# Performance work log

Hardware: AMD Instinct MI355X
Metric: run time of the kernel (lower is better)

## Reference

```python
import jax, jax.numpy as jnp
import numpy as np

NT, C, B, N, H, E = 32768, 128, 64, 512, 4, 524288  # total nodes, channels, graphs, nodes/graph, heads, edges
DH = C // H
EPS = 1e-5


def batchnorm(x, g, b):
    # BatchNorm1d over the node dimension (training-mode batch statistics)
    m = x.mean(axis=0)
    v = x.var(axis=0)
    return (x - m) * jax.lax.rsqrt(v + EPS) * g + b


def setup_inputs() -> dict:
    key = jax.random.key(0)
    ks = jax.random.split(key, 8)
    s = 1.0 / np.sqrt(C)
    return dict(
        x=jax.random.normal(ks[0], (NT, C), jnp.float32),
        edge_index=jax.random.randint(ks[1], (2, E), 0, NT, dtype=jnp.int32),
        Wc=jax.random.normal(ks[2], (C, C), jnp.float32) * s,
        bc=jnp.zeros((C,), jnp.float32),
        in_proj_w=jax.random.normal(ks[3], (3 * C, C), jnp.float32) * s,
        in_proj_b=jnp.zeros((3 * C,), jnp.float32),
        out_proj_w=jax.random.normal(ks[4], (C, C), jnp.float32) * s,
        out_proj_b=jnp.zeros((C,), jnp.float32),
        gn1=jnp.ones((C,), jnp.float32), bn1=jnp.zeros((C,), jnp.float32),
        gn2=jnp.ones((C,), jnp.float32), bn2=jnp.zeros((C,), jnp.float32),
        gn3=jnp.ones((C,), jnp.float32), bn3=jnp.zeros((C,), jnp.float32),
        Wm1=jax.random.normal(ks[5], (2 * C, C), jnp.float32) * s,
        bm1=jnp.zeros((2 * C,), jnp.float32),
        Wm2=jax.random.normal(ks[6], (C, 2 * C), jnp.float32) / np.sqrt(2 * C),
        bm2=jnp.zeros((C,), jnp.float32),
    )


def reference(x, edge_index, Wc, bc, in_proj_w, in_proj_b, out_proj_w, out_proj_b,
              gn1, bn1, gn2, bn2, gn3, bn3, Wm1, bm1, Wm2, bm2):
    # --- local branch: mean-aggregation message passing + linear + residual + BN ---
    src, dst = edge_index[0], edge_index[1]
    agg = jax.ops.segment_sum(x[src], dst, num_segments=NT)            # [NT, C]
    cnt = jax.ops.segment_sum(jnp.ones((E, 1), x.dtype), dst, num_segments=NT)
    agg = agg / jnp.maximum(cnt, 1.0)
    h_local = agg @ Wc.T + bc + x                                       # dropout p=0 -> no-op
    h_local = batchnorm(h_local, gn1, bn1)

    # --- global branch: to_dense_batch (equal-size graphs -> reshape) + MHA ---
    hd = x.reshape(B, N, C)
    qkv = hd @ in_proj_w.T + in_proj_b                                  # [B, N, 3C]
    q, k, v = jnp.split(qkv, 3, axis=-1)
    q = q.reshape(B, N, H, DH).transpose(0, 2, 1, 3)                    # [B, H, N, DH]
    k = k.reshape(B, N, H, DH).transpose(0, 2, 1, 3)
    v = v.reshape(B, N, H, DH).transpose(0, 2, 1, 3)
    scores = jnp.einsum('bhqd,bhkd->bhqk', q, k) / np.sqrt(DH)          # [B, H, N, N]
    attn = jax.nn.softmax(scores, axis=-1)
    o = jnp.einsum('bhqk,bhkd->bhqd', attn, v)                          # [B, H, N, DH]
    o = o.transpose(0, 2, 1, 3).reshape(B, N, C)
    h_attn = (o @ out_proj_w.T + out_proj_b).reshape(NT, C) + x
    h_attn = batchnorm(h_attn, gn2, bn2)

    # --- combine + MLP + final norm ---
    out = h_local + h_attn
    out = out + (jax.nn.relu(out @ Wm1.T + bm1) @ Wm2.T + bm2)
    return batchnorm(out, gn3, bn3)
```

## Files before the change

### kernel.cpp

```cpp
#include <hip/hip_runtime.h>
#include <cstddef>

#define NT    32768
#define CCH   128
#define BB    64
#define NNODE 512
#define NHEAD 4
#define DHEAD 32
#define EE    524288
#define EPS   1e-5f
#define MAXDEG 96
#define CURPAD 16
#define SSLOT  8
#define EGRP  2048
#define FILL0 2128

typedef unsigned short u16;
typedef unsigned int   u32;
typedef __attribute__((ext_vector_type(8))) short short8;
typedef __attribute__((ext_vector_type(4))) short short4v;
typedef __attribute__((ext_vector_type(4))) float f32x4;

__device__ __forceinline__ float b2f(u32 w) { return __uint_as_float(w << 16); }
__device__ __forceinline__ u16 f2b(float f) {
    u32 u = __float_as_uint(f);
    u += 0x7FFF + ((u >> 16) & 1);
    return (u16)(u >> 16);
}
__device__ __forceinline__ u32 cvtpk(float lo, float hi) {
    u32 r;
    asm("v_cvt_pk_bf16_f32 %0, %1, %2" : "=v"(r) : "v"(lo), "v"(hi));
    return r;
}
#if __has_builtin(__builtin_amdgcn_exp2f)
#define EXP2(x) __builtin_amdgcn_exp2f(x)
#else
#define EXP2(x) exp2f(x)
#endif
#define SCLOG2E (0.1767766952966369f * 1.4426950408889634f)

__global__ __launch_bounds__(256) void prep_kernel(const float* __restrict__ x,
                                                   const float* __restrict__ Wc,
                                                   const float* __restrict__ Wqkv,
                                                   const float* __restrict__ Wo,
                                                   const float* __restrict__ Wm1,
                                                   const float* __restrict__ Wm2,
                                                   u16* __restrict__ xb,
                                                   u16* __restrict__ Wcb,
                                                   u16* __restrict__ Wqkvb,
                                                   u16* __restrict__ Wob,
                                                   u16* __restrict__ Wm1b,
                                                   u16* __restrict__ Wm2b,
                                                   const float* __restrict__ bqkv,
                                                   float* __restrict__ bqs,
                                                   const int* __restrict__ ei,
                                                   int* __restrict__ cursor,
                                                   int* __restrict__ bucket) {
    int bid = blockIdx.x;
    if (bid >= FILL0) {
        int b2 = bid - FILL0;
        int k = b2 & 7;
        int g = b2 >> 3;
        int base_e = g * EGRP;
        for (int j = threadIdx.x; j < EGRP; j += 256) {
            int dst = ei[EE + base_e + j];
            if ((dst & 7) == k) {
                int src = ei[base_e + j];
                int pos = atomicAdd(cursor + dst * CURPAD, 1);
                if (pos < MAXDEG) bucket[dst * MAXDEG + pos] = src;
            }
        }
        return;
    }
    if (bid == 2120) {
        int t = threadIdx.x;
        if (t < 384) {
            float v = bqkv[t];
            if (t < 128) v *= SCLOG2E;
            bqs[t] = v;
        }
        return;
    }
    if (bid > 2120) return;
    int r = bid * 256 + threadIdx.x;
    const float* src; u16* dst; float qs = 1.0f;
    if (r < 524288) { src = x; dst = xb; }
    else if ((r -= 524288) < 2048) { src = Wc; dst = Wcb; }
    else if ((r -= 2048) < 6144) { src = Wqkv; dst = Wqkvb; if (r < 2048) qs = SCLOG2E; }
    else if ((r -= 6144) < 2048) { src = Wo; dst = Wob; }
    else if ((r -= 2048) < 4096) { src = Wm1; dst = Wm1b; }
    else { r -= 4096; src = Wm2; dst = Wm2b; }
    size_t base = (size_t)r * 8;
    float4 a = *(const float4*)(src + base);
    float4 b = *(const float4*)(src + base + 4);
    uint4 u;
    u.x = cvtpk(a.x * qs, a.y * qs);
    u.y = cvtpk(a.z * qs, a.w * qs);
    u.z = cvtpk(b.x * qs, b.y * qs);
    u.w = cvtpk(b.z * qs, b.w * qs);
    *(uint4*)(dst + base) = u;
}

struct GemmSmem {
    u16 As[128 * 32];
    u16 Bs[128 * 32];
    u16 Cs[4][16 * 72];
    float csum[128];
    float csq[128];
};

template <bool RELU, int RESID, bool STATS>
__device__ __forceinline__ void gemm_body(u16* __restrict__ As, u16* __restrict__ Bs,
                                          u16* __restrict__ Cs0, float* __restrict__ csum,
                                          float* __restrict__ csq,
                                          const u16* __restrict__ A,
                                          const u16* __restrict__ W,
                                          const float* __restrict__ bias,
                                          const u16* __restrict__ residb,
                                          u16* __restrict__ outb, int ostride,
                                          float* __restrict__ sum, float* __restrict__ sumsq,
                                          int slotbase, int m0, int K) {
    int tid = threadIdx.x;
    int lane = tid & 63, wave = tid >> 6;
    int wm = (wave & 1) * 64, wn = (wave >> 1) * 64;
    int l15 = lane & 15, l4 = lane >> 4;
    u16* Csw = Cs0 + wave * (16 * 72);

    if (STATS) {
        if (tid < 128) { csum[tid] = 0.f; csq[tid] = 0.f; }
    }

    f32x4 zero = {0.f, 0.f, 0.f, 0.f};
    f32x4 acc[4][4];
#pragma unroll
    for (int i = 0; i < 4; ++i)
#pragma unroll
        for (int j = 0; j < 4; ++j) acc[i][j] = zero;

    int srow = tid >> 2;
    int scol = (tid & 3) * 8;

    int kIter = K >> 5;
    uint4 a0 = *(const uint4*)(A + (size_t)(m0 + srow) * K + scol);
    uint4 a1 = *(const uint4*)(A + (size_t)(m0 + srow + 64) * K + scol);
    uint4 b0 = *(const uint4*)(W + (size_t)srow * K + scol);
    uint4 b1 = *(const uint4*)(W + (size_t)(srow + 64) * K + scol);
    for (int ki = 0; ki < kIter; ++ki) {
        if (ki) __syncthreads();
        *(uint4*)&As[srow * 32 + scol] = a0;
        *(uint4*)&As[(srow + 64) * 32 + scol] = a1;
        *(uint4*)&Bs[srow * 32 + scol] = b0;
        *(uint4*)&Bs[(srow + 64) * 32 + scol] = b1;
        if (ki + 1 < kIter) {
            int k0 = (ki + 1) * 32;
            a0 = *(const uint4*)(A + (size_t)(m0 + srow) * K + k0 + scol);
            a1 = *(const uint4*)(A + (size_t)(m0 + srow + 64) * K + k0 + scol);
            b0 = *(const uint4*)(W + (size_t)srow * K + k0 + scol);
            b1 = *(const uint4*)(W + (size_t)(srow + 64) * K + k0 + scol);
        }
        __syncthreads();
        short8 af[4], bf[4];
#pragma unroll
        for (int t = 0; t < 4; ++t) {
            af[t] = *(const short8*)&As[(wm + t * 16 + l15) * 32 + l4 * 8];
            bf[t] = *(const short8*)&Bs[(wn + t * 16 + l15) * 32 + l4 * 8];
        }
#pragma unroll
        for (int mt = 0; mt < 4; ++mt)
#pragma unroll
            for (int nt = 0; nt < 4; ++nt)
                acc[mt][nt] = __builtin_amdgcn_mfma_f32_16x16x32_bf16(af[mt], bf[nt], acc[mt][nt], 0, 0, 0);
    }

    float ps[4] = {0.f, 0.f, 0.f, 0.f};
    float pq[4] = {0.f, 0.f, 0.f, 0.f};
    int rl = lane >> 3;
    int cg = lane & 7;
#pragma unroll
    for (int mt = 0; mt < 4; ++mt) {
#pragma unroll
        for (int nt = 0; nt < 4; ++nt) {
            int lcol = wn + nt * 16 + l15;
            float bs = bias[lcol];
#pragma unroll
            for (int r = 0; r < 4; ++r) {
                int row = m0 + wm + mt * 16 + l4 * 4 + r;
                float v = acc[mt][nt][r] + bs;
                if (RESID == 2) v += b2f(residb[(size_t)row * 128 + lcol]);
                if (RELU) v = fmaxf(v, 0.0f);
                Csw[(l4 * 4 + r) * 72 + nt * 16 + l15] = f2b(v);
                if (STATS) { ps[nt] += v; pq[nt] += v * v; }
            }
        }
#pragma unroll
        for (int p = 0; p < 2; ++p) {
            int lrow = p * 8 + rl;
            uint4 wv = *(const uint4*)&Csw[lrow * 72 + cg * 8];
            int grow = m0 + wm + mt * 16 + lrow;
            *(uint4*)(outb + (size_t)grow * ostride + wn + cg * 8) = wv;
        }
    }
    if (STATS) {
#pragma unroll
        for (int nt = 0; nt < 4; ++nt) {
            atomicAdd(&csum[wn + nt * 16 + l15], ps[nt]);
            atomicAdd(&csq[wn + nt * 16 + l15], pq[nt]);
        }
        __syncthreads();
        if (tid < 128) {
            atomicAdd(sum + slotbase + tid, csum[tid]);
            atomicAdd(sumsq + slotbase + tid, csq[tid]);
        }
    }
}

__global__ __launch_bounds__(256) void gemm_qkv(const u16* __restrict__ xb,
                                                const u16* __restrict__ Wqkvb,
                                                const float* __restrict__ bqs,
                                                u16* __restrict__ qkvb) {
    __shared__ GemmSmem sm;
    int y = blockIdx.y;
    gemm_body<false, 0, false>(sm.As, sm.Bs, &sm.Cs[0][0], sm.csum, sm.csq,
                               xb, Wqkvb + (size_t)y * 16384, bqs + y * 128, nullptr,
                               qkvb + y * 128, 384, nullptr, nullptr, 0, blockIdx.x * 128, 128);
}

struct K3Smem {
    union {
        struct { u16 Ks[512 * 40]; u16 Vt[32 * 520]; } a;
        GemmSmem g;
    };
};

__global__ __launch_bounds__(256) void attn_gwc(const u16* __restrict__ qkv,
                                                u16* __restrict__ o,
                                                const int* __restrict__ bucket,
                                                const int* __restrict__ cursor,
                                                const u16* __restrict__ Wcb,
                                                const float* __restrict__ bc,
                                                const u16* __restrict__ xb,
                                                u16* __restrict__ aggb,
                                                u16* __restrict__ hlocb,
                                                float* __restrict__ sum1,
                                                float* __restrict__ sq1) {
    __shared__ __align__(16) K3Smem sm;
    int bid = blockIdx.x;
    int tid = threadIdx.x;

    if (bid < 256) {
        u16* Ks = sm.a.Ks;
        u16* Vt = sm.a.Vt;
        int b = bid >> 2, h = bid & 3;
        int lane = tid & 63, wave = tid >> 6;
        int quad = lane >> 4, l15 = lane & 15;

        const u16* kvbase = qkv + (size_t)b * 512 * 384 + 128 + h * 32;
        for (int idx = tid; idx < 2048; idx += 256) {
            int row = idx >> 2, c = idx & 3;
            *(uint4*)&Ks[row * 40 + c * 8] = *(const uint4*)(kvbase + (size_t)row * 384 + c * 8);
        }
        for (int idx = tid; idx < 2048; idx += 256) {
            int row = idx >> 2, c = idx & 3;
            uint4 u = *(const uint4*)(kvbase + 128 + (size_t)row * 384 + c * 8);
            u16 e[8];
            *(uint4*)e = u;
#pragma unroll
            for (int i = 0; i < 8; ++i) Vt[(c * 8 + i) * 520 + row] = e[i];
        }
        __syncthreads();

        f32x4 zero = {0.f, 0.f, 0.f, 0.f};
        for (int qt = 0; qt < 8; ++qt) {
            int qbase = wave * 128 + qt * 16;
            short8 qf = *(const short8*)(qkv + (size_t)(b * 512 + qbase + l15) * 384 + h * 32 + quad * 8);
            float lq = 0.f;
            f32x4 oa[2] = {zero, zero};

            for (int kv0 = 0; kv0 < 512; kv0 += 64) {
                f32x4 s[4];
#pragma unroll
                for (int t = 0; t < 4; ++t) {
                    short8 kb = *(const short8*)&Ks[(kv0 + t * 16 + l15) * 40 + quad * 8];
                    s[t] = __builtin_amdgcn_mfma_f32_16x16x32_bf16(kb, qf, zero, 0, 0, 0);
                }
                u32 ppw[2][4];
#pragma unroll
                for (int t = 0; t < 4; ++t) {
                    float p0 = EXP2(s[t][0]);
                    float p1 = EXP2(s[t][1]);
                    float p2 = EXP2(s[t][2]);
                    float p3 = EXP2(s[t][3]);
                    lq += (p0 + p1) + (p2 + p3);
                    ppw[t >> 1][(t & 1) * 2 + 0] = cvtpk(p0, p1);
                    ppw[t >> 1][(t & 1) * 2 + 1] = cvtpk(p2, p3);
                }
                short8 pps[2];
                pps[0] = *(const short8*)&ppw[0][0];
                pps[1] = *(const short8*)&ppw[1][0];
#pragma unroll
                for (int tp = 0; tp < 2; ++tp) {
                    int tb = kv0 + tp * 32;
#pragma unroll
                    for (int n = 0; n < 2; ++n) {
                        const u16* vrow = &Vt[(n * 16 + l15) * 520 + tb + quad * 4];
                        short4v va = *(const short4v*)vrow;
                        short4v vb2 = *(const short4v*)(vrow + 16);
                        short8 vv = {va.x, va.y, va.z, va.w, vb2.x, vb2.y, vb2.z, vb2.w};
                        oa[n] = __builtin_amdgcn_mfma_f32_16x16x32_bf16(pps[tp], vv, oa[n], 0, 0, 0);
                    }
                }
            }
            lq += __shfl_xor(lq, 16);
            lq += __shfl_xor(lq, 32);
            u16* op = o + (size_t)(b * 512 + qbase) * 128 + h * 32;
#pragma unroll
            for (int r = 0; r < 4; ++r) {
                float Lr = __shfl(lq, quad * 4 + r);
                float inv = 1.0f / Lr;
#pragma unroll
                for (int n = 0; n < 2; ++n)
                    op[(quad * 4 + r) * 128 + n * 16 + l15] = f2b(oa[n][r] * inv);
            }
        }
        return;
    }

    int m0 = (bid - 256) * 128;

    {
        int (*srcs)[MAXDEG] = reinterpret_cast<int (*)[MAXDEG]>(sm.g.As);
        int ln = tid >> 4;
        int c8 = tid & 15;
        const u16* xp = xb + c8 * 8;
        for (int pass = 0; pass < 8; ++pass) {
            int n = pass * 16 + ln;
            int gn = m0 + n;
            int d = min(cursor[gn * CURPAD], MAXDEG);
            for (int j = c8; j < d; j += 16) srcs[ln][j] = bucket[gn * MAXDEG + j];
            __syncthreads();
            float s[8] = {0.f, 0.f, 0.f, 0.f, 0.f, 0.f, 0.f, 0.f};
            for (int base = 0; base < d; base += 8) {
                uint4 w[8];
#pragma unroll
                for (int u = 0; u < 8; ++u) {
                    int jj = base + u;
                    int idx = srcs[ln][jj < d ? jj : 0];
                    w[u] = *(const uint4*)(xp + (size_t)idx * CCH);
                }
#pragma unroll
                for (int u = 0; u < 8; ++u) {
                    if (base + u >= d) { w[u].x = 0; w[u].y = 0; w[u].z = 0; w[u].w = 0; }
                    s[0] += b2f(w[u].x & 0xffffu);
                    s[1] += b2f(w[u].x >> 16);
                    s[2] += b2f(w[u].y & 0xffffu);
                    s[3] += b2f(w[u].y >> 16);
                    s[4] += b2f(w[u].z & 0xffffu);
                    s[5] += b2f(w[u].z >> 16);
                    s[6] += b2f(w[u].w & 0xffffu);
                    s[7] += b2f(w[u].w >> 16);
                }
            }
            float inv = 1.0f / fmaxf((float)d, 1.0f);
            uint4 out;
            out.x = cvtpk(s[0] * inv, s[1] * inv);
            out.y = cvtpk(s[2] * inv, s[3] * inv);
            out.z = cvtpk(s[4] * inv, s[5] * inv);
            out.w = cvtpk(s[6] * inv, s[7] * inv);
            *(uint4*)(aggb + (size_t)gn * CCH + c8 * 8) = out;
            __syncthreads();
        }
    }
    __syncthreads();

    gemm_body<false, 2, true>(sm.g.As, sm.g.Bs, &sm.g.Cs[0][0], sm.g.csum, sm.g.csq,
                              aggb, Wcb, bc, xb, hlocb, 128, sum1, sq1,
                              ((bid - 256) & (SSLOT - 1)) << 7, m0, 128);
}

__global__ __launch_bounds__(256) void gemm_wo(const u16* __restrict__ ob,
                                               const u16* __restrict__ Wob,
                                               const float* __restrict__ bo,
                                               const u16* __restrict__ xb,
                                               u16* __restrict__ t2b,
                                               float* __restrict__ sum2, float* __restrict__ sq2) {
    __shared__ GemmSmem sm;
    gemm_body<false, 2, true>(sm.As, sm.Bs, &sm.Cs[0][0], sm.csum, sm.csq,
                              ob, Wob, bo, xb, t2b, 128, sum2, sq2,
                              (blockIdx.x & (SSLOT - 1)) << 7, blockIdx.x * 128, 128);
}

__global__ __launch_bounds__(256) void gemm_mlp2(const u16* __restrict__ hidb,
                                                 const u16* __restrict__ Wm2b,
                                                 const float* __restrict__ bm2,
                                                 const u16* __restrict__ shb,
                                                 u16* __restrict__ out2b,
                                                 float* __restrict__ sum3, float* __restrict__ sq3) {
    __shared__ GemmSmem sm;
    gemm_body<false, 2, true>(sm.As, sm.Bs, &sm.Cs[0][0], sm.csum, sm.csq,
                              hidb, Wm2b, bm2, shb, out2b, 128, sum3, sq3,
                              (blockIdx.x & (SSLOT - 1)) << 7, blockIdx.x * 128, 256);
}

__global__ __launch_bounds__(256) void gemm_m1c(const u16* __restrict__ hlocb,
                                                const u16* __restrict__ t2b,
                                                const float* __restrict__ sum1,
                                                const float* __restrict__ sq1,
                                                const float* __restrict__ g1,
                                                const float* __restrict__ bt1,
                                                const float* __restrict__ sum2,
                                                const float* __restrict__ sq2,
                                                const float* __restrict__ g2,
                                                const float* __restrict__ bt2,
                                                u16* __restrict__ shb,
                                                const u16* __restrict__ Wm1b,
                                                const float* __restrict__ bm1,
                                                u16* __restrict__ hidb) {
    __shared__ u16 As[128 * 32];
    __shared__ u16 Bs[128 * 32];
    __shared__ u16 Cs[4][16 * 72];
    __shared__ float AF1[128], BF1[128], AF2[128], BF2[128];
    int tid = threadIdx.x;
    {
        int c = tid & 127;
        const float* sm = (tid < 128) ? sum1 : sum2;
        const float* sq = (tid < 128) ? sq1 : sq2;
        const float* g  = (tid < 128) ? g1 : g2;
        const float* bt = (tid < 128) ? bt1 : bt2;
        float s = 0.f, q = 0.f;
#pragma unroll
        for (int sl = 0; sl < SSLOT; ++sl) { s += sm[sl * 128 + c]; q += sq[sl * 128 + c]; }
        float m = s * (1.0f / NT);
        float v = q * (1.0f / NT) - m * m;
        float a = g[c] * rsqrtf(v + EPS);
        if (tid < 128) { AF1[c] = a; BF1[c] = bt[c] - m * a; }
        else           { AF2[c] = a; BF2[c] = bt[c] - m * a; }
    }
    int m0 = blockIdx.x * 128, n0 = blockIdx.y * 128;
    int lane = tid & 63, wave = tid >> 6;
    int wm = (wave & 1) * 64, wn = (wave >> 1) * 64;
    int l15 = lane & 15, l4 = lane >> 4;

    f32x4 zero = {0.f, 0.f, 0.f, 0.f};
    f32x4 acc[4][4];
#pragma unroll
    for (int i = 0; i < 4; ++i)
#pragma unroll
        for (int j = 0; j < 4; ++j) acc[i][j] = zero;

    int srow = tid >> 2;
    int scol = (tid & 3) * 8;
    bool wr = (blockIdx.y == 0);

    uint4 h0 = *(const uint4*)(hlocb + (size_t)(m0 + srow) * 128 + scol);
    uint4 h1 = *(const uint4*)(hlocb + (size_t)(m0 + srow + 64) * 128 + scol);
    uint4 t0 = *(const uint4*)(t2b + (size_t)(m0 + srow) * 128 + scol);
    uint4 t1 = *(const uint4*)(t2b + (size_t)(m0 + srow + 64) * 128 + scol);
    uint4 b0 = *(const uint4*)(Wm1b + (size_t)(n0 + srow) * 128 + scol);
    uint4 b1 = *(const uint4*)(Wm1b + (size_t)(n0 + srow + 64) * 128 + scol);
    __syncthreads();
    for (int ki = 0; ki < 4; ++ki) {
        int k0 = ki * 32;
        if (ki) __syncthreads();
        uint4 c0, c1;
        {
            const u32 hw[4] = {h0.x, h0.y, h0.z, h0.w};
            const u32 tw[4] = {t0.x, t0.y, t0.z, t0.w};
            u32 ow[4];
#pragma unroll
            for (int p = 0; p < 4; ++p) {
                int cc = k0 + scol + p * 2;
                float v0 = AF1[cc] * b2f(hw[p] & 0xffffu) + BF1[cc] + AF2[cc] * b2f(tw[p] & 0xffffu) + BF2[cc];
                float v1 = AF1[cc + 1] * b2f(hw[p] >> 16) + BF1[cc + 1] + AF2[cc + 1] * b2f(tw[p] >> 16) + BF2[cc + 1];
                ow[p] = cvtpk(v0, v1);
            }
            c0.x = ow[0]; c0.y = ow[1]; c0.z = ow[2]; c0.w = ow[3];
        }
        {
            const u32 hw[4] = {h1.x, h1.y, h1.z, h1.w};
            const u32 tw[4] = {t1.x, t1.y, t1.z, t1.w};
            u32 ow[4];
#pragma unroll
            for (int p = 0; p < 4; ++p) {
                int cc = k0 + scol + p * 2;
                float v0 = AF1[cc] * b2f(hw[p] & 0xffffu) + BF1[cc] + AF2[cc] * b2f(tw[p] & 0xffffu) + BF2[cc];
                float v1 = AF1[cc + 1] * b2f(hw[p] >> 16) + BF1[cc + 1] + AF2[cc + 1] * b2f(tw[p] >> 16) + BF2[cc + 1];
                ow[p] = cvtpk(v0, v1);
            }
            c1.x = ow[0]; c1.y = ow[1]; c1.z = ow[2]; c1.w = ow[3];
        }
        *(uint4*)&As[srow * 32 + scol] = c0;
        *(uint4*)&As[(srow + 64) * 32 + scol] = c1;
        *(uint4*)&Bs[srow * 32 + scol] = b0;
        *(uint4*)&Bs[(srow + 64) * 32 + scol] = b1;
        if (wr) {
            *(uint4*)(shb + (size_t)(m0 + srow) * 128 + k0 + scol) = c0;
            *(uint4*)(shb + (size_t)(m0 + srow + 64) * 128 + k0 + scol) = c1;
        }
        if (ki < 3) {
            int kn = k0 + 32;
            h0 = *(const uint4*)(hlocb + (size_t)(m0 + srow) * 128 + kn + scol);
            h1 = *(const uint4*)(hlocb + (size_t)(m0 + srow + 64) * 128 + kn + scol);
            t0 = *(const uint4*)(t2b + (size_t)(m0 + srow) * 128 + kn + scol);
            t1 = *(const uint4*)(t2b + (size_t)(m0 + srow + 64) * 128 + kn + scol);
            b0 = *(const uint4*)(Wm1b + (size_t)(n0 + srow) * 128 + kn + scol);
            b1 = *(const uint4*)(Wm1b + (size_t)(n0 + srow + 64) * 128 + kn + scol);
        }
        __syncthreads();
        short8 af[4], bf[4];
#pragma unroll
        for (int t = 0; t < 4; ++t) {
            af[t] = *(const short8*)&As[(wm + t * 16 + l15) * 32 + l4 * 8];
            bf[t] = *(const short8*)&Bs[(wn + t * 16 + l15) * 32 + l4 * 8];
        }
#pragma unroll
        for (int mt = 0; mt < 4; ++mt)
#pragma unroll
            for (int nt = 0; nt < 4; ++nt)
                acc[mt][nt] = __builtin_amdgcn_mfma_f32_16x16x32_bf16(af[mt], bf[nt], acc[mt][nt], 0, 0, 0);
    }

    int rl = lane >> 3;
    int cg = lane & 7;
#pragma unroll
    for (int mt = 0; mt < 4; ++mt) {
#pragma unroll
        for (int nt = 0; nt < 4; ++nt) {
            int col = n0 + wn + nt * 16 + l15;
            float bs = bm1[col];
#pragma unroll
            for (int r = 0; r < 4; ++r) {
                float v = fmaxf(acc[mt][nt][r] + bs, 0.0f);
                Cs[wave][(l4 * 4 + r) * 72 + nt * 16 + l15] = f2b(v);
            }
        }
#pragma unroll
        for (int p = 0; p < 2; ++p) {
            int lrow = p * 8 + rl;
            uint4 wv = *(const uint4*)&Cs[wave][lrow * 72 + cg * 8];
            int grow = m0 + wm + mt * 16 + lrow;
            *(uint4*)(hidb + (size_t)grow * 256 + n0 + wn + cg * 8) = wv;
        }
    }
}

__global__ __launch_bounds__(256) void final_bn(const u16* __restrict__ X,
                                                const float* __restrict__ sum3,
                                                const float* __restrict__ sq3,
                                                const float* __restrict__ g3,
                                                const float* __restrict__ bt3,
                                                float* __restrict__ outp) {
    __shared__ float A3[128], B3[128];
    int t = threadIdx.x;
    if (t < 128) {
        float s = 0.f, q = 0.f;
#pragma unroll
        for (int sl = 0; sl < SSLOT; ++sl) { s += sum3[sl * 128 + t]; q += sq3[sl * 128 + t]; }
        float m = s * (1.0f / NT);
        float v = q * (1.0f / NT) - m * m;
        float a = g3[t] * rsqrtf(v + EPS);
        A3[t] = a;
        B3[t] = bt3[t] - m * a;
    }
    __syncthreads();
    int i8 = blockIdx.x * 256 + t;
    size_t i = (size_t)i8 * 8;
    int c = (int)(i & (CCH - 1));
    uint4 u = *(const uint4*)(X + i);
    float x[8];
    x[0] = b2f(u.x & 0xffffu); x[1] = b2f(u.x >> 16);
    x[2] = b2f(u.y & 0xffffu); x[3] = b2f(u.y >> 16);
    x[4] = b2f(u.z & 0xffffu); x[5] = b2f(u.z >> 16);
    x[6] = b2f(u.w & 0xffffu); x[7] = b2f(u.w >> 16);
    float4 o0, o1;
    o0.x = A3[c + 0] * x[0] + B3[c + 0];
    o0.y = A3[c + 1] * x[1] + B3[c + 1];
    o0.z = A3[c + 2] * x[2] + B3[c + 2];
    o0.w = A3[c + 3] * x[3] + B3[c + 3];
    o1.x = A3[c + 4] * x[4] + B3[c + 4];
    o1.y = A3[c + 5] * x[5] + B3[c + 5];
    o1.z = A3[c + 6] * x[6] + B3[c + 6];
    o1.w = A3[c + 7] * x[7] + B3[c + 7];
    *(float4*)(outp + i) = o0;
    *(float4*)(outp + i + 4) = o1;
}

extern "C" void kernel_launch(void* const* d_in, const int* in_sizes, int n_in,
                              void* d_out, int out_size, void* d_ws, size_t ws_size,
                              hipStream_t stream) {
    const float* x    = (const float*)d_in[0];
    const int*   ei   = (const int*)d_in[1];
    const float* Wc   = (const float*)d_in[2];
    const float* bc   = (const float*)d_in[3];
    const float* Wqkv = (const float*)d_in[4];
    const float* bqkv = (const float*)d_in[5];
    const float* Wo   = (const float*)d_in[6];
    const float* bo   = (const float*)d_in[7];
    const float* gn1  = (const float*)d_in[8];
    const float* bn1b = (const float*)d_in[9];
    const float* gn2  = (const float*)d_in[10];
    const float* bn2b = (const float*)d_in[11];
    const float* gn3  = (const float*)d_in[12];
    const float* bn3b = (const float*)d_in[13];
    const float* Wm1  = (const float*)d_in[14];
    const float* bm1  = (const float*)d_in[15];
    const float* Wm2  = (const float*)d_in[16];
    const float* bm2  = (const float*)d_in[17];
    float* outp = (float*)d_out;

    char* w = (char*)d_ws;
    const size_t MB = 1024 * 1024;
    u16* xb    = (u16*)(w);
    u16* hlocb = (u16*)(w + 8 * MB);
    u16* t2b   = (u16*)(w + 16 * MB);
    u16* out2b = (u16*)(w + 24 * MB);
    u16* qkvb  = (u16*)(w + 32 * MB);
    u16* hidb  = (u16*)(w + 56 * MB);
    u16* shb   = (u16*)(w + 72 * MB);
    int* bucket = (int*)(w + 80 * MB);
    int* cursor = (int*)(w + 92 * MB);
    float* stats = (float*)(w + 94 * MB);
    u16* Wcb   = (u16*)(w + 95 * MB);
    u16* Wqkvb = Wcb + 16384;
    u16* Wob   = Wqkvb + 49152;
    u16* Wm1b  = Wob + 16384;
    u16* Wm2b  = Wm1b + 32768;
    u16* ob    = (u16*)(w + 96 * MB);
    float* sum1 = stats;                  float* sq1 = stats + 1024;
    float* sum2 = stats + 2048;           float* sq2 = stats + 3072;
    float* sum3 = stats + 4096;           float* sq3 = stats + 5120;
    float* bqs  = stats + 6144;

    hipMemsetAsync(cursor, 0, 2 * MB + 7 * 1024 * 4, stream);

    prep_kernel<<<FILL0 + 2048, 256, 0, stream>>>(x, Wc, Wqkv, Wo, Wm1, Wm2,
                                                  xb, Wcb, Wqkvb, Wob, Wm1b, Wm2b,
                                                  bqkv, bqs, ei, cursor, bucket);

    {
        dim3 g(NT / 128, 3);
        gemm_qkv<<<g, 256, 0, stream>>>(xb, Wqkvb, bqs, qkvb);
    }

    attn_gwc<<<512, 256, 0, stream>>>(qkvb, ob, bucket, cursor, Wcb, bc, xb,
                                      shb , hlocb, sum1, sq1);

    gemm_wo<<<NT / 128, 256, 0, stream>>>(ob, Wob, bo, xb, t2b, sum2, sq2);

    {
        dim3 g(NT / 128, 2);
        gemm_m1c<<<g, 256, 0, stream>>>(hlocb, t2b, sum1, sq1, gn1, bn1b,
                                        sum2, sq2, gn2, bn2b, shb, Wm1b, bm1, hidb);
    }

    gemm_mlp2<<<NT / 128, 256, 0, stream>>>(hidb, Wm2b, bm2, shb, out2b, sum3, sq3);

    final_bn<<<NT * CCH / 8 / 256, 256, 0, stream>>>(out2b, sum3, sq3, gn3, bn3b, outp);
}
```

Baseline: 220.1 us.

## Split Wc GEMM out of attention kernel and widen attention blocks to 512 threads

The attention-plus-gather kernel now runs 512 threads per block. Attention blocks split the 512 queries over 8 waves instead of 4, and gather blocks process 32 nodes per pass. The Wc linear layer that used to run at the tail of the gather blocks moves into a combined GEMM launch with the Wo projection, using blockIdx.y to pick the operands. This is meant to balance the mixed attention/gather grid, raise wave count per block, and run the two 128x128 GEMMs as one larger grid, at the cost of writing and re-reading the aggregate buffer through global memory.

```diff
diff --git a/kernel.cpp b/kernel.cpp
--- a/kernel.cpp
+++ b/kernel.cpp
@@ -225,25 +225,20 @@
                                qkvb + y * 128, 384, nullptr, nullptr, 0, blockIdx.x * 128, 128);
 }
 
-struct K3Smem {
+struct AGSmem {
     union {
         struct { u16 Ks[512 * 40]; u16 Vt[32 * 520]; } a;
-        GemmSmem g;
+        int srcs[32][MAXDEG];
     };
 };
 
-__global__ __launch_bounds__(256) void attn_gwc(const u16* __restrict__ qkv,
-                                                u16* __restrict__ o,
-                                                const int* __restrict__ bucket,
-                                                const int* __restrict__ cursor,
-                                                const u16* __restrict__ Wcb,
-                                                const float* __restrict__ bc,
-                                                const u16* __restrict__ xb,
-                                                u16* __restrict__ aggb,
-                                                u16* __restrict__ hlocb,
-                                                float* __restrict__ sum1,
-                                                float* __restrict__ sq1) {
-    __shared__ __align__(16) K3Smem sm;
+__global__ __launch_bounds__(512) void attn_gath(const u16* __restrict__ qkv,
+                                                 u16* __restrict__ o,
+                                                 const int* __restrict__ bucket,
+                                                 const int* __restrict__ cursor,
+                                                 const u16* __restrict__ xb,
+                                                 u16* __restrict__ aggb) {
+    __shared__ __align__(16) AGSmem sm;
     int bid = blockIdx.x;
     int tid = threadIdx.x;
 
@@ -255,11 +250,11 @@
         int quad = lane >> 4, l15 = lane & 15;
 
         const u16* kvbase = qkv + (size_t)b * 512 * 384 + 128 + h * 32;
-        for (int idx = tid; idx < 2048; idx += 256) {
+        for (int idx = tid; idx < 2048; idx += 512) {
             int row = idx >> 2, c = idx & 3;
             *(uint4*)&Ks[row * 40 + c * 8] = *(const uint4*)(kvbase + (size_t)row * 384 + c * 8);
         }
-        for (int idx = tid; idx < 2048; idx += 256) {
+        for (int idx = tid; idx < 2048; idx += 512) {
             int row = idx >> 2, c = idx & 3;
             uint4 u = *(const uint4*)(kvbase + 128 + (size_t)row * 384 + c * 8);
             u16 e[8];
@@ -270,8 +265,8 @@
         __syncthreads();
 
         f32x4 zero = {0.f, 0.f, 0.f, 0.f};
-        for (int qt = 0; qt < 8; ++qt) {
-            int qbase = wave * 128 + qt * 16;
+        for (int qt = 0; qt < 4; ++qt) {
+            int qbase = wave * 64 + qt * 16;
             short8 qf = *(const short8*)(qkv + (size_t)(b * 512 + qbase + l15) * 384 + h * 32 + quad * 8);
             float lq = 0.f;
             f32x4 oa[2] = {zero, zero};
@@ -325,18 +320,16 @@
         return;
     }
 
-    int m0 = (bid - 256) * 128;
-
     {
-        int (*srcs)[MAXDEG] = reinterpret_cast<int (*)[MAXDEG]>(sm.g.As);
+        int m0 = (bid - 256) * 128;
         int ln = tid >> 4;
         int c8 = tid & 15;
         const u16* xp = xb + c8 * 8;
-        for (int pass = 0; pass < 8; ++pass) {
-            int n = pass * 16 + ln;
+        for (int pass = 0; pass < 4; ++pass) {
+            int n = pass * 32 + ln;
             int gn = m0 + n;
             int d = min(cursor[gn * CURPAD], MAXDEG);
-            for (int j = c8; j < d; j += 16) srcs[ln][j] = bucket[gn * MAXDEG + j];
+            for (int j = c8; j < d; j += 16) sm.srcs[ln][j] = bucket[gn * MAXDEG + j];
             __syncthreads();
             float s[8] = {0.f, 0.f, 0.f, 0.f, 0.f, 0.f, 0.f, 0.f};
             for (int base = 0; base < d; base += 8) {
@@ -344,7 +337,7 @@
 #pragma unroll
                 for (int u = 0; u < 8; ++u) {
                     int jj = base + u;
-                    int idx = srcs[ln][jj < d ? jj : 0];
+                    int idx = sm.srcs[ln][jj < d ? jj : 0];
                     w[u] = *(const uint4*)(xp + (size_t)idx * CCH);
                 }
 #pragma unroll
@@ -370,23 +363,32 @@
             __syncthreads();
         }
     }
-    __syncthreads();
-
-    gemm_body<false, 2, true>(sm.g.As, sm.g.Bs, &sm.g.Cs[0][0], sm.g.csum, sm.g.csq,
-                              aggb, Wcb, bc, xb, hlocb, 128, sum1, sq1,
-                              ((bid - 256) & (SSLOT - 1)) << 7, m0, 128);
-}
-
-__global__ __launch_bounds__(256) void gemm_wo(const u16* __restrict__ ob,
-                                               const u16* __restrict__ Wob,
-                                               const float* __restrict__ bo,
-                                               const u16* __restrict__ xb,
-                                               u16* __restrict__ t2b,
-                                               float* __restrict__ sum2, float* __restrict__ sq2) {
+}
+
+__global__ __launch_bounds__(256) void gemm_wc_wo(const u16* __restrict__ aggb,
+                                                  const u16* __restrict__ Wcb,
+                                                  const float* __restrict__ bc,
+                                                  const u16* __restrict__ ob,
+                                                  const u16* __restrict__ Wob,
+                                                  const float* __restrict__ bo,
+                                                  const u16* __restrict__ xb,
+                                                  u16* __restrict__ hlocb,
+                                                  u16* __restrict__ t2b,
+                                                  float* __restrict__ sum1, float* __restrict__ sq1,
+                                                  float* __restrict__ sum2, float* __restrict__ sq2) {
     __shared__ GemmSmem sm;
+    bool wo = (blockIdx.y != 0);
+    int m0 = blockIdx.x * 128;
+    int slotbase = (blockIdx.x & (SSLOT - 1)) << 7;
     gemm_body<false, 2, true>(sm.As, sm.Bs, &sm.Cs[0][0], sm.csum, sm.csq,
-                              ob, Wob, bo, xb, t2b, 128, sum2, sq2,
-                              (blockIdx.x & (SSLOT - 1)) << 7, blockIdx.x * 128, 128);
+                              wo ? ob : aggb,
+                              wo ? Wob : Wcb,
+                              wo ? bo : bc,
+                              xb,
+                              wo ? t2b : hlocb, 128,
+                              wo ? sum2 : sum1,
+                              wo ? sq2 : sq1,
+                              slotbase, m0, 128);
 }
 
 __global__ __launch_bounds__(256) void gemm_mlp2(const u16* __restrict__ hidb,
@@ -641,10 +643,13 @@
         gemm_qkv<<<g, 256, 0, stream>>>(xb, Wqkvb, bqs, qkvb);
     }
 
-    attn_gwc<<<512, 256, 0, stream>>>(qkvb, ob, bucket, cursor, Wcb, bc, xb,
-                                      shb , hlocb, sum1, sq1);
-
-    gemm_wo<<<NT / 128, 256, 0, stream>>>(ob, Wob, bo, xb, t2b, sum2, sq2);
+    attn_gath<<<512, 512, 0, stream>>>(qkvb, ob, bucket, cursor, xb, shb );
+
+    {
+        dim3 g(NT / 128, 2);
+        gemm_wc_wo<<<g, 256, 0, stream>>>(shb, Wcb, bc, ob, Wob, bo, xb,
+                                          hlocb, t2b, sum1, sq1, sum2, sq2);
+    }
 
     {
         dim3 g(NT / 128, 2);
```

Result: faster. 210.6 us (-4.3%).
